# Kernel tuning notes

Measured on AMD Instinct MI355X. Metric: run time of the kernel, lower is better.

The kernel has to match this reference:

```python
import jax, jax.numpy as jnp
import numpy as np

E, D, F = 8, 1024, 4096
G = 2048  # tokens per expert


def setup_inputs() -> dict:
    key = jax.random.key(0)
    k1, k2, k3, k4 = jax.random.split(key, 4)
    scale = 1.0 / np.sqrt(D)
    return {
        "routed_in_egD": jax.random.normal(k1, (E * G, D), dtype=jnp.float32),
        "moe_w_in_eD_F": jax.random.normal(k2, (E * D, F), dtype=jnp.float32) * scale,
        "moe_w_swiglu_eD_F": jax.random.normal(k3, (E * D, F), dtype=jnp.float32) * scale,
        "moe_w_out_eF_D": jax.random.normal(k4, (E * F, D), dtype=jnp.float32) * (1.0 / np.sqrt(F)),
    }


def reference(routed_in_egD, moe_w_in_eD_F, moe_w_swiglu_eD_F, moe_w_out_eF_D):
    w_in = moe_w_in_eD_F.reshape(E, D, F)        # [e, D, F]
    w_swiglu = moe_w_swiglu_eD_F.reshape(E, D, F)
    w_out = moe_w_out_eF_D.reshape(E, F, D)      # [e, F, D]
    x = routed_in_egD.reshape(E, -1, D)          # [e, g, D]
    middle = jnp.einsum("egd,edf->egf", x, w_in)
    gate = jnp.einsum("egd,edf->egf", x, w_swiglu)
    hidden = jax.nn.silu(middle) * gate          # fused SwiGLU
    out = jnp.einsum("egf,efd->egd", hidden, w_out)
    return out.reshape(-1, D)
```

## Files before the change

kernel.cpp:

```cpp
#include <hip/hip_runtime.h>
#include <hip/hip_bf16.h>

#define E_ 8
#define D_ 1024
#define F_ 4096
#define G_ 2048

typedef __attribute__((ext_vector_type(8))) short bf16x8;
typedef __attribute__((ext_vector_type(4))) float f32x4;
typedef __attribute__((ext_vector_type(8))) unsigned short u16x8;
typedef unsigned short u16;
typedef unsigned int u32;

__device__ __forceinline__ u16 f2bf(float f) {
  u32 u = __float_as_uint(f);
  u = (u + 0x7fffu + ((u >> 16) & 1u)) >> 16;
  return (u16)u;
}

__device__ __forceinline__ void gld_lds16(const void* g, void* l) {
  __builtin_amdgcn_global_load_lds(
      (const __attribute__((address_space(1))) u32*)g,
      (__attribute__((address_space(3))) u32*)l, 16, 0, 0);
}

__global__ __launch_bounds__(256) void k_cvt(const float* __restrict__ in,
                                             u16* __restrict__ out, int n8) {
  int i = blockIdx.x * 256 + threadIdx.x;
  if (i >= n8) return;
  const float4* p = (const float4*)in + (size_t)i * 2;
  float4 a = p[0], b = p[1];
  u16x8 o;
  o[0] = f2bf(a.x); o[1] = f2bf(a.y); o[2] = f2bf(a.z); o[3] = f2bf(a.w);
  o[4] = f2bf(b.x); o[5] = f2bf(b.y); o[6] = f2bf(b.z); o[7] = f2bf(b.w);
  *(u16x8*)(out + (size_t)i * 8) = o;
}

__global__ __launch_bounds__(256) void k_tcvt(const float* __restrict__ in,
                                              u16* __restrict__ out, int R, int C) {
  __shared__ __align__(16) u16 Tt[64 * 72];
  size_t base = (size_t)blockIdx.z * (size_t)R * (size_t)C;
  in += base; out += base;
  const int c0 = blockIdx.x * 64, r0 = blockIdx.y * 64;
  const int tid = threadIdx.x;
  {
    const int cq = tid & 15, rr = tid >> 4;
    const float* ip = in + (size_t)(r0 + rr) * C + c0 + cq * 4;
#pragma unroll
    for (int i = 0; i < 4; i++) {
      float4 v = *(const float4*)(ip + (size_t)(16 * i) * C);
      const int r = rr + 16 * i, c = cq * 4;
      Tt[(c + 0) * 72 + r] = f2bf(v.x);
      Tt[(c + 1) * 72 + r] = f2bf(v.y);
      Tt[(c + 2) * 72 + r] = f2bf(v.z);
      Tt[(c + 3) * 72 + r] = f2bf(v.w);
    }
  }
  __syncthreads();
  {
    const int rq = tid & 7, cc0 = tid >> 3;
#pragma unroll
    for (int i = 0; i < 2; i++) {
      const int cc = cc0 + 32 * i;
      u16x8 v = *(const u16x8*)(Tt + cc * 72 + rq * 8);
      *(u16x8*)(out + (size_t)(c0 + cc) * R + r0 + rq * 8) = v;
    }
  }
}

__global__ __launch_bounds__(256) void k_mlp1(const u16* __restrict__ X,
                                              const u16* __restrict__ W1t,
                                              const u16* __restrict__ W2t,
                                              u16* __restrict__ H) {
  __shared__ __align__(16) u16 As[128 * 32];
  __shared__ __align__(16) u16 B1s[64 * 32];
  __shared__ __align__(16) u16 B2s[64 * 32];
  const int e = blockIdx.z;
  const u16* A  = X   + (size_t)e * G_ * D_;
  const u16* B1 = W1t + (size_t)e * F_ * D_;
  const u16* B2 = W2t + (size_t)e * F_ * D_;
  u16* Hp = H + (size_t)e * G_ * F_;
  const int bm = blockIdx.y * 128, bn = blockIdx.x * 64;
  const int tid = threadIdx.x, wave = tid >> 6, lane = tid & 63;
  const int wm = (wave >> 1) * 64, wn = (wave & 1) * 32;
  const int quad = lane >> 4, l16 = lane & 15;

  const int ea0 = wave * 512 + lane * 8;
  const int ra0 = ea0 >> 5, ra1 = ra0 + 64;
  const int qs0 = (ea0 >> 3) & 3;
  const int ca0 = (qs0 ^ ((ra0 >> 1) & 3)) << 3;
  const int fco = ((quad ^ ((l16 >> 1) & 3)) << 3);

  f32x4 acc1[4][2], acc2[4][2];
#pragma unroll
  for (int i = 0; i < 4; i++)
#pragma unroll
    for (int j = 0; j < 2; j++) {
      acc1[i][j] = f32x4{0.f, 0.f, 0.f, 0.f};
      acc2[i][j] = f32x4{0.f, 0.f, 0.f, 0.f};
    }

  for (int k0 = 0; k0 < D_; k0 += 32) {
    gld_lds16(A  + (size_t)(bm + ra0) * D_ + k0 + ca0, (char*)As  + wave * 1024);
    gld_lds16(A  + (size_t)(bm + ra1) * D_ + k0 + ca0, (char*)As  + (wave + 4) * 1024);
    gld_lds16(B1 + (size_t)(bn + ra0) * D_ + k0 + ca0, (char*)B1s + wave * 1024);
    gld_lds16(B2 + (size_t)(bn + ra0) * D_ + k0 + ca0, (char*)B2s + wave * 1024);
    __syncthreads();
    bf16x8 af[4], b1f[2], b2f[2];
#pragma unroll
    for (int i = 0; i < 4; i++)
      af[i] = *(const bf16x8*)(As + (wm + i * 16 + l16) * 32 + fco);
#pragma unroll
    for (int j = 0; j < 2; j++) {
      b1f[j] = *(const bf16x8*)(B1s + (wn + j * 16 + l16) * 32 + fco);
      b2f[j] = *(const bf16x8*)(B2s + (wn + j * 16 + l16) * 32 + fco);
    }
#pragma unroll
    for (int i = 0; i < 4; i++)
#pragma unroll
      for (int j = 0; j < 2; j++) {
        acc1[i][j] = __builtin_amdgcn_mfma_f32_16x16x32_bf16(af[i], b1f[j], acc1[i][j], 0, 0, 0);
        acc2[i][j] = __builtin_amdgcn_mfma_f32_16x16x32_bf16(af[i], b2f[j], acc2[i][j], 0, 0, 0);
      }
    __syncthreads();
  }
#pragma unroll
  for (int i = 0; i < 4; i++)
#pragma unroll
    for (int j = 0; j < 2; j++)
#pragma unroll
      for (int r = 0; r < 4; r++) {
        float m = acc1[i][j][r], g = acc2[i][j][r];
        float h = (m / (1.f + __expf(-m))) * g;
        int row = bm + wm + i * 16 + quad * 4 + r;
        int col = bn + wn + j * 16 + l16;
        Hp[(size_t)row * F_ + col] = f2bf(h);
      }
}

__global__ __launch_bounds__(256) void k_mlp2(const u16* __restrict__ H,
                                              const u16* __restrict__ W3t,
                                              float* __restrict__ O) {
  __shared__ __align__(16) u16 As[128 * 32];
  __shared__ __align__(16) u16 Bs[128 * 32];
  const int e = blockIdx.z;
  const u16* A = H   + (size_t)e * G_ * F_;
  const u16* B = W3t + (size_t)e * D_ * F_;
  float* C = O + (size_t)e * G_ * D_;
  const int bm = blockIdx.y * 128, bn = blockIdx.x * 128;
  const int tid = threadIdx.x, wave = tid >> 6, lane = tid & 63;
  const int wm = (wave >> 1) * 64, wn = (wave & 1) * 64;
  const int quad = lane >> 4, l16 = lane & 15;

  const int ea0 = wave * 512 + lane * 8;
  const int ra0 = ea0 >> 5, ra1 = ra0 + 64;
  const int qs0 = (ea0 >> 3) & 3;
  const int ca0 = (qs0 ^ ((ra0 >> 1) & 3)) << 3;
  const int fco = ((quad ^ ((l16 >> 1) & 3)) << 3);

  f32x4 acc[4][4];
#pragma unroll
  for (int i = 0; i < 4; i++)
#pragma unroll
    for (int j = 0; j < 4; j++) acc[i][j] = f32x4{0.f, 0.f, 0.f, 0.f};

  for (int k0 = 0; k0 < F_; k0 += 32) {
    gld_lds16(A + (size_t)(bm + ra0) * F_ + k0 + ca0, (char*)As + wave * 1024);
    gld_lds16(A + (size_t)(bm + ra1) * F_ + k0 + ca0, (char*)As + (wave + 4) * 1024);
    gld_lds16(B + (size_t)(bn + ra0) * F_ + k0 + ca0, (char*)Bs + wave * 1024);
    gld_lds16(B + (size_t)(bn + ra1) * F_ + k0 + ca0, (char*)Bs + (wave + 4) * 1024);
    __syncthreads();
    bf16x8 af[4], bf[4];
#pragma unroll
    for (int i = 0; i < 4; i++) {
      af[i] = *(const bf16x8*)(As + (wm + i * 16 + l16) * 32 + fco);
      bf[i] = *(const bf16x8*)(Bs + (wn + i * 16 + l16) * 32 + fco);
    }
#pragma unroll
    for (int i = 0; i < 4; i++)
#pragma unroll
      for (int j = 0; j < 4; j++)
        acc[i][j] = __builtin_amdgcn_mfma_f32_16x16x32_bf16(af[i], bf[j], acc[i][j], 0, 0, 0);
    __syncthreads();
  }
#pragma unroll
  for (int i = 0; i < 4; i++)
#pragma unroll
    for (int j = 0; j < 4; j++)
#pragma unroll
      for (int r = 0; r < 4; r++) {
        int row = bm + wm + i * 16 + quad * 4 + r;
        int col = bn + wn + j * 16 + l16;
        C[(size_t)row * D_ + col] = acc[i][j][r];
      }
}

extern "C" void kernel_launch(void* const* d_in, const int* in_sizes, int n_in,
                              void* d_out, int out_size, void* d_ws, size_t ws_size,
                              hipStream_t stream) {
  const float* x  = (const float*)d_in[0];
  const float* w1 = (const float*)d_in[1];
  const float* w2 = (const float*)d_in[2];
  const float* w3 = (const float*)d_in[3];
  float* out = (float*)d_out;
  char* ws = (char*)d_ws;

  u16* Xb  = (u16*)(ws);
  u16* W1t = (u16*)(ws + (size_t)32 * 1024 * 1024);
  u16* W2t = (u16*)(ws + (size_t)96 * 1024 * 1024);
  u16* Hb  = (u16*)(ws + (size_t)160 * 1024 * 1024);
  u16* W3t = (u16*)(ws);

  k_cvt<<<dim3((E_ * G_ * D_ / 8 + 255) / 256), dim3(256), 0, stream>>>(
      x, Xb, E_ * G_ * D_ / 8);
  k_tcvt<<<dim3(F_ / 64, D_ / 64, E_), dim3(256), 0, stream>>>(w1, W1t, D_, F_);
  k_tcvt<<<dim3(F_ / 64, D_ / 64, E_), dim3(256), 0, stream>>>(w2, W2t, D_, F_);
  k_mlp1<<<dim3(F_ / 64, G_ / 128, E_), dim3(256), 0, stream>>>(Xb, W1t, W2t, Hb);
  k_tcvt<<<dim3(D_ / 64, F_ / 64, E_), dim3(256), 0, stream>>>(w3, W3t, F_, D_);
  k_mlp2<<<dim3(D_ / 128, G_ / 128, E_), dim3(256), 0, stream>>>(Hb, W3t, out);
}
```

Before: 974.7 us.

## Remap GEMM block indices for XCD-aware L2 locality and vectorize transpose LDS writes

Both GEMM kernels now launch a 1D grid and decode block IDs so that blocks landing on the same XCD (round-robin by block id mod 8) work on neighbouring tiles of the same expert. Each XCD's L2 therefore sees more reuse of A and B tiles. The transpose-convert kernel now loads four rows per thread and packs four bf16 values into one ushort4 LDS store, with a 68-element padded stride, instead of scalar 16-bit stores. The index math is more complex and relies on the assumed XCD dispatch order to deliver the locality.

```diff
diff --git a/kernel.cpp b/kernel.cpp
--- a/kernel.cpp
+++ b/kernel.cpp
@@ -38,32 +38,37 @@
 
 __global__ __launch_bounds__(256) void k_tcvt(const float* __restrict__ in,
                                               u16* __restrict__ out, int R, int C) {
-  __shared__ __align__(16) u16 Tt[64 * 72];
+  __shared__ __align__(16) u16 Tt[64 * 68];
   size_t base = (size_t)blockIdx.z * (size_t)R * (size_t)C;
   in += base; out += base;
   const int c0 = blockIdx.x * 64, r0 = blockIdx.y * 64;
   const int tid = threadIdx.x;
   {
-    const int cq = tid & 15, rr = tid >> 4;
-    const float* ip = in + (size_t)(r0 + rr) * C + c0 + cq * 4;
+    const int cq = tid & 15, rb = tid >> 4;
+    float4 v[4];
+    const float* ip = in + (size_t)(r0 + rb * 4) * C + c0 + cq * 4;
+#pragma unroll
+    for (int rr = 0; rr < 4; rr++) v[rr] = *(const float4*)(ip + (size_t)rr * C);
 #pragma unroll
     for (int i = 0; i < 4; i++) {
-      float4 v = *(const float4*)(ip + (size_t)(16 * i) * C);
-      const int r = rr + 16 * i, c = cq * 4;
-      Tt[(c + 0) * 72 + r] = f2bf(v.x);
-      Tt[(c + 1) * 72 + r] = f2bf(v.y);
-      Tt[(c + 2) * 72 + r] = f2bf(v.z);
-      Tt[(c + 3) * 72 + r] = f2bf(v.w);
+      ushort4 pk;
+      pk.x = f2bf((&v[0].x)[i]); pk.y = f2bf((&v[1].x)[i]);
+      pk.z = f2bf((&v[2].x)[i]); pk.w = f2bf((&v[3].x)[i]);
+      *(ushort4*)(Tt + (cq * 4 + i) * 68 + rb * 4) = pk;
     }
   }
   __syncthreads();
   {
-    const int rq = tid & 7, cc0 = tid >> 3;
-#pragma unroll
-    for (int i = 0; i < 2; i++) {
-      const int cc = cc0 + 32 * i;
-      u16x8 v = *(const u16x8*)(Tt + cc * 72 + rq * 8);
-      *(u16x8*)(out + (size_t)(c0 + cc) * R + r0 + rq * 8) = v;
+    const int rq = tid & 7, cc = tid >> 3;
+#pragma unroll
+    for (int it = 0; it < 2; it++) {
+      const int c = cc + 32 * it;
+      ushort4 a = *(const ushort4*)(Tt + c * 68 + rq * 8);
+      ushort4 b = *(const ushort4*)(Tt + c * 68 + rq * 8 + 4);
+      u16x8 o;
+      o[0] = a.x; o[1] = a.y; o[2] = a.z; o[3] = a.w;
+      o[4] = b.x; o[5] = b.y; o[6] = b.z; o[7] = b.w;
+      *(u16x8*)(out + (size_t)(c0 + c) * R + r0 + rq * 8) = o;
     }
   }
 }
@@ -75,12 +80,18 @@
   __shared__ __align__(16) u16 As[128 * 32];
   __shared__ __align__(16) u16 B1s[64 * 32];
   __shared__ __align__(16) u16 B2s[64 * 32];
-  const int e = blockIdx.z;
+  const int l = blockIdx.x;
+  const int xcd = l & 7, s = l >> 3;
+  const int wp = s & 31, pl = s >> 5;
+  const int pg = pl * 8 + xcd;
+  const int e = pg >> 5, pe = pg & 31;
+  const int bm = ((pe >> 3) * 4 + (wp >> 3)) * 128;
+  const int bn = ((pe & 7) * 8 + (wp & 7)) * 64;
+
   const u16* A  = X   + (size_t)e * G_ * D_;
   const u16* B1 = W1t + (size_t)e * F_ * D_;
   const u16* B2 = W2t + (size_t)e * F_ * D_;
   u16* Hp = H + (size_t)e * G_ * F_;
-  const int bm = blockIdx.y * 128, bn = blockIdx.x * 64;
   const int tid = threadIdx.x, wave = tid >> 6, lane = tid & 63;
   const int wm = (wave >> 1) * 64, wn = (wave & 1) * 32;
   const int quad = lane >> 4, l16 = lane & 15;
@@ -143,11 +154,17 @@
                                               float* __restrict__ O) {
   __shared__ __align__(16) u16 As[128 * 32];
   __shared__ __align__(16) u16 Bs[128 * 32];
-  const int e = blockIdx.z;
+  const int l = blockIdx.x;
+  const int xcd = l & 7, s = l >> 3;
+  const int wp = s & 15, pl = s >> 4;
+  const int pg = pl * 8 + xcd;
+  const int e = pg >> 3, pe = pg & 7;
+  const int bm = ((pe >> 1) * 4 + (wp >> 2)) * 128;
+  const int bn = ((pe & 1) * 4 + (wp & 3)) * 128;
+
   const u16* A = H   + (size_t)e * G_ * F_;
   const u16* B = W3t + (size_t)e * D_ * F_;
   float* C = O + (size_t)e * G_ * D_;
-  const int bm = blockIdx.y * 128, bn = blockIdx.x * 128;
   const int tid = threadIdx.x, wave = tid >> 6, lane = tid & 63;
   const int wm = (wave >> 1) * 64, wn = (wave & 1) * 64;
   const int quad = lane >> 4, l16 = lane & 15;
@@ -215,7 +232,7 @@
       x, Xb, E_ * G_ * D_ / 8);
   k_tcvt<<<dim3(F_ / 64, D_ / 64, E_), dim3(256), 0, stream>>>(w1, W1t, D_, F_);
   k_tcvt<<<dim3(F_ / 64, D_ / 64, E_), dim3(256), 0, stream>>>(w2, W2t, D_, F_);
-  k_mlp1<<<dim3(F_ / 64, G_ / 128, E_), dim3(256), 0, stream>>>(Xb, W1t, W2t, Hb);
+  k_mlp1<<<dim3(8192), dim3(256), 0, stream>>>(Xb, W1t, W2t, Hb);
   k_tcvt<<<dim3(D_ / 64, F_ / 64, E_), dim3(256), 0, stream>>>(w3, W3t, F_, D_);
-  k_mlp2<<<dim3(D_ / 128, G_ / 128, E_), dim3(256), 0, stream>>>(Hb, W3t, out);
-}
+  k_mlp2<<<dim3(1024), dim3(256), 0, stream>>>(Hb, W3t, out);
+}
```

Result: slower. 995.2 us (+2.1%).
